# Kernel tuning notes

Measured on AMD Instinct MI355X. Metric: run time of the kernel, lower is better.

The kernel has to match this reference:

```python
import jax, jax.numpy as jnp
import numpy as np

NEG_SLOPE = 0.2  # DGL GATConv default leaky_relu slope


def gat_conv(x, src, dst, W, attn_l, attn_r, bias, res_W):
    """DGL GATConv (eval mode, residual=True with linear res_fc, bias).
    x: [N, F_in]; src/dst: [E]; W: [F_in, H*D]; attn_l/r: [H, D];
    bias: [H*D]; res_W: [F_in, H*D]. Returns [N, H, D]."""
    N = x.shape[0]
    H, D = attn_l.shape
    feat = (x @ W).reshape(N, H, D)
    el = jnp.sum(feat * attn_l, axis=-1)  # [N, H]
    er = jnp.sum(feat * attn_r, axis=-1)  # [N, H]
    e = jax.nn.leaky_relu(el[src] + er[dst], NEG_SLOPE)  # [E, H]
    # edge softmax over incoming edges of each dst node (numerically stable)
    m = jnp.full((N, H), -jnp.inf, dtype=e.dtype).at[dst].max(e)
    ex = jnp.exp(e - m[dst])
    s = jnp.zeros((N, H), dtype=e.dtype).at[dst].add(ex)
    alpha = ex / s[dst]  # [E, H]
    # scatter-aggregate messages alpha * feat[src] into dst
    rst = jnp.zeros((N, H, D), dtype=x.dtype).at[dst].add(alpha[:, :, None] * feat[src])
    rst = rst + (x @ res_W).reshape(N, H, D) + bias.reshape(1, H, D)
    return rst


def setup_inputs() -> dict:
    key = jax.random.key(0)
    N, E, F_IN, HID, OUT, H = 20000, 320000, 128, 128, 128, 4
    ks = jax.random.split(key, 32)
    ki = iter(range(32))

    def rn(shape, scale=0.05):
        return jax.random.normal(ks[next(ki)], shape, dtype=jnp.float32) * scale

    inp = {
        "n_feat": jax.random.normal(ks[next(ki)], (N, F_IN), dtype=jnp.float32),
        "src": jax.random.randint(ks[next(ki)], (E,), 0, N, dtype=jnp.int32),
        "dst": jax.random.randint(ks[next(ki)], (E,), 0, N, dtype=jnp.int32),
        # input GATConv: F_IN -> H x HID
        "W0": rn((F_IN, H * HID)), "al0": rn((H, HID)), "ar0": rn((H, HID)),
        "b0": rn((H * HID,)), "rW0": rn((F_IN, H * HID)),
        "DW0": rn((H * HID, HID)), "Db0": rn((HID,)),
        # middle GATConv: HID -> H x HID
        "W1": rn((HID, H * HID)), "al1": rn((H, HID)), "ar1": rn((H, HID)),
        "b1": rn((H * HID,)), "rW1": rn((HID, H * HID)),
        "DW1": rn((H * HID, HID)), "Db1": rn((HID,)),
        # output GATConv: HID -> H x OUT
        "W2": rn((HID, H * OUT)), "al2": rn((H, OUT)), "ar2": rn((H, OUT)),
        "b2": rn((H * OUT,)), "rW2": rn((HID, H * OUT)),
    }
    return inp


def reference(n_feat, src, dst,
              W0, al0, ar0, b0, rW0, DW0, Db0,
              W1, al1, ar1, b1, rW1, DW1, Db1,
              W2, al2, ar2, b2, rW2):
    N = n_feat.shape[0]
    relu = jax.nn.relu
    # input GAT block
    h = relu(gat_conv(n_feat, src, dst, W0, al0, ar0, b0, rW0))  # [N, H, HID]
    h = relu(h.reshape(N, -1) @ DW0 + Db0)                        # [N, HID]
    # middle GAT block
    h = relu(gat_conv(h, src, dst, W1, al1, ar1, b1, rW1))
    h = relu(h.reshape(N, -1) @ DW1 + Db1)
    # output GAT + head-mean + graph max pooling (single graph)
    h = relu(gat_conv(h, src, dst, W2, al2, ar2, b2, rW2))        # [N, H, OUT]
    h = relu(jnp.mean(h, axis=-2))                                 # [N, OUT]
    return jnp.max(h, axis=0, keepdims=True)                       # [1, OUT]
```

## Files before the change

kernel.cpp:

```cpp
#include <hip/hip_runtime.h>
#include <hip/hip_bf16.h>


typedef __attribute__((ext_vector_type(8))) short bf16x8;
typedef __attribute__((ext_vector_type(4))) float f32x4;
typedef __hip_bfloat16 bf16_t;

__device__ __forceinline__ unsigned int pack_bf16(float lo, float hi) {
  return (((unsigned int)__bfloat16_as_ushort(__float2bfloat16(hi))) << 16) |
         (unsigned int)__bfloat16_as_ushort(__float2bfloat16(lo));
}

__device__ __forceinline__ void gload_lds16(const void* g, void* l) {
  __builtin_amdgcn_global_load_lds(
      (const __attribute__((address_space(1))) void*)g,
      (__attribute__((address_space(3))) void*)l, 16, 0, 0);
}

__global__ __launch_bounds__(256) void mega_prep(
    const float* __restrict__ W0, const float* __restrict__ rW0,
    const float* __restrict__ W1, const float* __restrict__ rW1,
    const float* __restrict__ W2, const float* __restrict__ rW2,
    const float* __restrict__ DW0, const float* __restrict__ DW1,
    const float* __restrict__ al0, const float* __restrict__ ar0,
    const float* __restrict__ al1, const float* __restrict__ ar1,
    const float* __restrict__ al2, const float* __restrict__ ar2,
    const float* __restrict__ n_feat, bf16_t* __restrict__ wts,
    float* __restrict__ ALR, bf16_t* __restrict__ xbf,
    int* __restrict__ counts, float* __restrict__ d_out_f, int N) {
  __shared__ float tile[32][33];
  int b = blockIdx.x, tid = threadIdx.x;
  int r = tid >> 5, c = tid & 31;

  if (b < 384) {
    int mat = b >> 6;
    int t = b & 63;
    int kt = t >> 4, nt = t & 15;
    int L = mat >> 1, isR = mat & 1;
    const float* S = (L == 0) ? (isR ? rW0 : W0)
                   : (L == 1) ? (isR ? rW1 : W1) : (isR ? rW2 : W2);
    bf16_t* D = wts + L * 131072 + isR * 65536;
#pragma unroll
    for (int rr = 0; rr < 4; rr++)
      tile[r + rr * 8][c] = S[(kt * 32 + r + rr * 8) * 512 + nt * 32 + c];
    __syncthreads();
#pragma unroll
    for (int rr = 0; rr < 4; rr++)
      D[(nt * 32 + r + rr * 8) * 128 + kt * 32 + c] =
          __float2bfloat16(tile[c][r + rr * 8]);
  } else if (b < 512) {
    int i = b - 384;
    int mat = i >> 6;
    int t = i & 63;
    int kt = t & 15, nt = t >> 4;
    const float* S = mat ? DW1 : DW0;
    bf16_t* D = wts + 393216 + mat * 65536;
#pragma unroll
    for (int rr = 0; rr < 4; rr++)
      tile[r + rr * 8][c] = S[(kt * 32 + r + rr * 8) * 128 + nt * 32 + c];
    __syncthreads();
#pragma unroll
    for (int rr = 0; rr < 4; rr++)
      D[(nt * 32 + r + rr * 8) * 512 + kt * 32 + c] =
          __float2bfloat16(tile[c][r + rr * 8]);
  } else if (b < 524) {
    int idx = (b - 512) * 256 + tid;
    if (idx < 3072) {
      int L = idx >> 10;
      int k = (idx >> 3) & 127;
      int cc = idx & 7;
      int h = cc & 3;
      const float* W = (L == 0) ? W0 : (L == 1) ? W1 : W2;
      const float* a = (cc < 4) ? ((L == 0) ? al0 : (L == 1) ? al1 : al2)
                                : ((L == 0) ? ar0 : (L == 1) ? ar1 : ar2);
      float s = 0.f;
      for (int d = 0; d < 128; d++) s += W[k * 512 + h * 128 + d] * a[h * 128 + d];
      ALR[idx] = s;
    }
  } else if (b < 3024) {
    int i = ((b - 524) * 256 + tid) * 4;
    if (i < N * 128) {
      float4 v = *(const float4*)(n_feat + i);
      xbf[i + 0] = __float2bfloat16(v.x);
      xbf[i + 1] = __float2bfloat16(v.y);
      xbf[i + 2] = __float2bfloat16(v.z);
      xbf[i + 3] = __float2bfloat16(v.w);
    }
  } else {
    for (int i = tid; i < N; i += 256) counts[i] = 0;
    if (tid < 128) d_out_f[tid] = 0.f;
  }
}

__global__ __launch_bounds__(256) void gemm128el(
    const bf16_t* __restrict__ A, const bf16_t* __restrict__ Bt,
    const float* __restrict__ ALRl, bf16_t* __restrict__ C,
    float* __restrict__ el, float* __restrict__ er, int M, int ldc, int K) {
  __shared__ bf16_t As[128 * 64];
  __shared__ bf16_t Bs[128 * 64];
  int tid = threadIdx.x;
  int rowBase = blockIdx.y * 128;

  if (blockIdx.x == 8) {
    float* sALR = (float*)As;
#pragma unroll
    for (int j = 0; j < 4; j++) sALR[tid * 4 + j] = ALRl[tid * 4 + j];
    __syncthreads();
    int row = rowBase + (tid >> 1);
    int half = tid & 1;
    if (row < M) {
      const bf16_t* xr = A + (size_t)row * K + half * 64;
      float s[8] = {};
#pragma unroll
      for (int g = 0; g < 8; g++) {
        bf16x8 v = *(const bf16x8*)(xr + g * 8);
#pragma unroll
        for (int e = 0; e < 8; e++) {
          float f = __uint_as_float(((unsigned int)(unsigned short)v[e]) << 16);
          const float* Ak = sALR + (half * 64 + g * 8 + e) * 8;
#pragma unroll
          for (int cc = 0; cc < 8; cc++) s[cc] += f * Ak[cc];
        }
      }
#pragma unroll
      for (int cc = 0; cc < 8; cc++) s[cc] += __shfl_xor(s[cc], 1);
      if (half == 0)
        *(float4*)(el + row * 4) = make_float4(s[0], s[1], s[2], s[3]);
      else
        *(float4*)(er + row * 4) = make_float4(s[4], s[5], s[6], s[7]);
    }
    return;
  }

  int lane = tid & 63, wave = tid >> 6;
  int q = lane >> 4, r16 = lane & 15;
  int wm = (wave >> 1) * 64, wn = (wave & 1) * 64;
  int colBase = blockIdx.x * 128;

  f32x4 acc[4][4] = {};

  for (int k0 = 0; k0 < K; k0 += 64) {
#pragma unroll
    for (int p = 0; p < 4; p++) {
      int slotb = (wave * 4 + p) * 64;
      int s = slotb + lane;
      int r = s >> 3;
      int c = (s & 7) ^ (r & 7);
      int gr = rowBase + r;
      if (gr > M - 1) gr = M - 1;
      gload_lds16(A + (size_t)gr * K + k0 + c * 8, (char*)As + (size_t)slotb * 16);
      gload_lds16(Bt + (size_t)(colBase + r) * K + k0 + c * 8,
                  (char*)Bs + (size_t)slotb * 16);
    }
    __syncthreads();
#pragma unroll
    for (int ks = 0; ks < 64; ks += 32) {
      int koff = ks >> 3;
      bf16x8 af[4], bfr[4];
#pragma unroll
      for (int i = 0; i < 4; i++) {
        int R = wm + i * 16 + r16;
        int slot = R * 8 + ((q + koff) ^ (R & 7));
        af[i] = *(const bf16x8*)((const char*)As + (size_t)slot * 16);
      }
#pragma unroll
      for (int j = 0; j < 4; j++) {
        int R = wn + j * 16 + r16;
        int slot = R * 8 + ((q + koff) ^ (R & 7));
        bfr[j] = *(const bf16x8*)((const char*)Bs + (size_t)slot * 16);
      }
#pragma unroll
      for (int i = 0; i < 4; i++)
#pragma unroll
        for (int j = 0; j < 4; j++)
          acc[i][j] = __builtin_amdgcn_mfma_f32_16x16x32_bf16(af[i], bfr[j], acc[i][j], 0, 0, 0);
    }
    __syncthreads();
  }

  int odd = lane & 1;
  int colb0 = r16 & ~1;
#pragma unroll
  for (int i = 0; i < 4; i++) {
#pragma unroll
    for (int r = 0; r < 4; r++) {
      int row = rowBase + wm + i * 16 + q * 4 + r;
#pragma unroll
      for (int jp = 0; jp < 2; jp++) {
        float a0 = acc[i][2 * jp][r];
        float a1 = acc[i][2 * jp + 1][r];
        float p0 = __shfl_xor(a0, 1);
        float p1 = __shfl_xor(a1, 1);
        float lo = odd ? p1 : a0;
        float hi = odd ? a1 : p0;
        int col = colBase + wn + (2 * jp + odd) * 16 + colb0;
        if (row < M)
          *(unsigned int*)(C + (size_t)row * ldc + col) = pack_bf16(lo, hi);
      }
    }
  }
}

__global__ __launch_bounds__(256) void mfma_gemm64(
    const bf16_t* __restrict__ A, const bf16_t* __restrict__ Bt,
    const float* __restrict__ bias, bf16_t* __restrict__ C,
    int M, int ldc, int K) {
  __shared__ bf16_t As[64 * 64];
  __shared__ bf16_t Bs[64 * 64];
  int tid = threadIdx.x;
  int lane = tid & 63, wave = tid >> 6;
  int q = lane >> 4, r16 = lane & 15;
  int wm = (wave >> 1) * 32, wn = (wave & 1) * 32;
  int rowBase = blockIdx.y * 64, colBase = blockIdx.x * 64;

  f32x4 acc[2][2] = {};

  for (int k0 = 0; k0 < K; k0 += 64) {
#pragma unroll
    for (int p = 0; p < 2; p++) {
      int slotb = (wave * 2 + p) * 64;
      int s = slotb + lane;
      int r = s >> 3;
      int c = (s & 7) ^ (r & 7);
      int gr = rowBase + r;
      if (gr > M - 1) gr = M - 1;
      gload_lds16(A + (size_t)gr * K + k0 + c * 8, (char*)As + (size_t)slotb * 16);
      gload_lds16(Bt + (size_t)(colBase + r) * K + k0 + c * 8,
                  (char*)Bs + (size_t)slotb * 16);
    }
    __syncthreads();
#pragma unroll
    for (int ks = 0; ks < 64; ks += 32) {
      int koff = ks >> 3;
      bf16x8 af[2], bfr[2];
#pragma unroll
      for (int i = 0; i < 2; i++) {
        int R = wm + i * 16 + r16;
        int slot = R * 8 + ((q + koff) ^ (R & 7));
        af[i] = *(const bf16x8*)((const char*)As + (size_t)slot * 16);
      }
#pragma unroll
      for (int j = 0; j < 2; j++) {
        int R = wn + j * 16 + r16;
        int slot = R * 8 + ((q + koff) ^ (R & 7));
        bfr[j] = *(const bf16x8*)((const char*)Bs + (size_t)slot * 16);
      }
#pragma unroll
      for (int i = 0; i < 2; i++)
#pragma unroll
        for (int j = 0; j < 2; j++)
          acc[i][j] = __builtin_amdgcn_mfma_f32_16x16x32_bf16(af[i], bfr[j], acc[i][j], 0, 0, 0);
    }
    __syncthreads();
  }

  int odd = lane & 1;
  int colb0 = r16 & ~1;
#pragma unroll
  for (int i = 0; i < 2; i++) {
#pragma unroll
    for (int r = 0; r < 4; r++) {
      int row = rowBase + wm + i * 16 + q * 4 + r;
      float a0 = acc[i][0][r];
      float a1 = acc[i][1][r];
      float p0 = __shfl_xor(a0, 1);
      float p1 = __shfl_xor(a1, 1);
      float lo = odd ? p1 : a0;
      float hi = odd ? a1 : p0;
      int col = colBase + wn + odd * 16 + colb0;
      if (row < M) {
        float o0 = fmaxf(lo + bias[col], 0.f);
        float o1 = fmaxf(hi + bias[col + 1], 0.f);
        *(unsigned int*)(C + (size_t)row * ldc + col) = pack_bf16(o0, o1);
      }
    }
  }
}

__global__ __launch_bounds__(256) void count_kernel(const int* __restrict__ dst,
                                                    int* __restrict__ counts, int E) {
  int i = blockIdx.x * blockDim.x + threadIdx.x;
  if (i < E) atomicAdd(&counts[dst[i]], 1);
}

__global__ __launch_bounds__(1024) void scan_kernel(const int* __restrict__ counts,
                                                    int* __restrict__ row_ptr,
                                                    int* __restrict__ cursor, int N) {
  __shared__ int sums[1024];
  int t = threadIdx.x;
  int chunk = (N + 1023) / 1024;
  int begin = t * chunk;
  int end = begin + chunk;
  if (end > N) end = N;
  int s = 0;
  for (int i = begin; i < end; i++) s += counts[i];
  sums[t] = s;
  __syncthreads();
  for (int off = 1; off < 1024; off <<= 1) {
    int v = (t >= off) ? sums[t - off] : 0;
    __syncthreads();
    sums[t] += v;
    __syncthreads();
  }
  int run = (t == 0) ? 0 : sums[t - 1];
  for (int i = begin; i < end; i++) {
    row_ptr[i] = run;
    cursor[i] = run;
    run += counts[i];
  }
  if (t == 1023) row_ptr[N] = sums[1023];
}

__global__ __launch_bounds__(256) void scatter_kernel(
    const int* __restrict__ src, const int* __restrict__ dst,
    int* __restrict__ cursor, int* __restrict__ edge_src, int E) {
  int i = blockIdx.x * blockDim.x + threadIdx.x;
  if (i < E) {
    int d = dst[i];
    int pos = atomicAdd(&cursor[d], 1);
    edge_src[pos] = src[i];
  }
}

__global__ __launch_bounds__(256) void gat_agg_kernel(
    const bf16_t* __restrict__ fused,
    const float* __restrict__ el, const float* __restrict__ er,
    const float* __restrict__ bias, const int* __restrict__ row_ptr,
    const int* __restrict__ edge_src, bf16_t* __restrict__ out, int N) {
  int n = blockIdx.x;
  int h = threadIdx.x >> 6;
  int l = threadIdx.x & 63;
  int g = l >> 3, t = l & 7;
  int start = row_ptr[n];
  int deg = row_ptr[n + 1] - start;
  float er_nh = er[n * 4 + h];

  float acc[16] = {};
  float ssum = 0.f;
  const bf16_t* fbase = fused + h * 128 + t * 16;
  for (int i = g; i < deg; i += 8) {
    int s = edge_src[start + i];
    float e = el[s * 4 + h] + er_nh;
    e = (e > 0.f) ? e : 0.2f * e;
    float w = __expf(e);
    ssum += w;
    const bf16_t* fp = fbase + (size_t)s * 1024;
    uint4 f0 = *(const uint4*)(fp);
    uint4 f1 = *(const uint4*)(fp + 8);
    unsigned int u[8] = {f0.x, f0.y, f0.z, f0.w, f1.x, f1.y, f1.z, f1.w};
#pragma unroll
    for (int j = 0; j < 8; j++) {
      acc[2 * j] += w * __uint_as_float(u[j] << 16);
      acc[2 * j + 1] += w * __uint_as_float(u[j] & 0xffff0000u);
    }
  }
#pragma unroll
  for (int off = 8; off <= 32; off <<= 1) {
    ssum += __shfl_xor(ssum, off);
#pragma unroll
    for (int d = 0; d < 16; d++) acc[d] += __shfl_xor(acc[d], off);
  }

  if (g == 0) {
    float inv = (deg > 0) ? 1.f / ssum : 0.f;
    const bf16_t* rp = fused + (size_t)n * 1024 + 512 + h * 128 + t * 16;
    uint4 r0 = *(const uint4*)(rp);
    uint4 r1 = *(const uint4*)(rp + 8);
    unsigned int ru[8] = {r0.x, r0.y, r0.z, r0.w, r1.x, r1.y, r1.z, r1.w};
    const float* bp = bias + h * 128 + t * 16;
    unsigned int ow[8];
#pragma unroll
    for (int j = 0; j < 8; j++) {
      float o0 = fmaxf(acc[2 * j] * inv + __uint_as_float(ru[j] << 16) + bp[2 * j], 0.f);
      float o1 = fmaxf(acc[2 * j + 1] * inv + __uint_as_float(ru[j] & 0xffff0000u) + bp[2 * j + 1], 0.f);
      ow[j] = pack_bf16(o0, o1);
    }
    bf16_t* op = out + (size_t)n * 512 + h * 128 + t * 16;
    *(uint4*)(op) = make_uint4(ow[0], ow[1], ow[2], ow[3]);
    *(uint4*)(op + 8) = make_uint4(ow[4], ow[5], ow[6], ow[7]);
  }
}

__global__ __launch_bounds__(128) void pool_kernel(const bf16_t* __restrict__ g,
                                                   float* __restrict__ out, int N) {
  int d = threadIdx.x;
  float mx = 0.f;
  for (int n = blockIdx.x; n < N; n += gridDim.x) {
    const bf16_t* p = g + (size_t)n * 512 + d;
    float v = 0.25f * (__bfloat162float(p[0]) + __bfloat162float(p[128]) +
                       __bfloat162float(p[256]) + __bfloat162float(p[384]));
    mx = fmaxf(mx, v);
  }
  atomicMax((int*)out + d, __float_as_int(mx));
}

extern "C" void kernel_launch(void* const* d_in, const int* in_sizes, int n_in,
                              void* d_out, int out_size, void* d_ws, size_t ws_size,
                              hipStream_t stream) {
  const float* n_feat = (const float*)d_in[0];
  const int* src = (const int*)d_in[1];
  const int* dst = (const int*)d_in[2];
  const float* W0 = (const float*)d_in[3];
  const float* al0 = (const float*)d_in[4];
  const float* ar0 = (const float*)d_in[5];
  const float* b0 = (const float*)d_in[6];
  const float* rW0 = (const float*)d_in[7];
  const float* DW0 = (const float*)d_in[8];
  const float* Db0 = (const float*)d_in[9];
  const float* W1 = (const float*)d_in[10];
  const float* al1 = (const float*)d_in[11];
  const float* ar1 = (const float*)d_in[12];
  const float* b1 = (const float*)d_in[13];
  const float* rW1 = (const float*)d_in[14];
  const float* DW1 = (const float*)d_in[15];
  const float* Db1 = (const float*)d_in[16];
  const float* W2 = (const float*)d_in[17];
  const float* al2 = (const float*)d_in[18];
  const float* ar2 = (const float*)d_in[19];
  const float* b2 = (const float*)d_in[20];
  const float* rW2 = (const float*)d_in[21];

  const int N = in_sizes[0] / 128;
  const int E = in_sizes[1];

  bf16_t* xbf = (bf16_t*)d_ws;
  bf16_t* fusedFR = xbf + (size_t)N * 128;
  bf16_t* outC = fusedFR + (size_t)N * 1024;
  bf16_t* denseD = outC + (size_t)N * 512;
  bf16_t* wts = denseD + (size_t)N * 128;
  float* ALR = (float*)(wts + 524288);
  float* el = ALR + 3072;
  float* er = el + (size_t)N * 4;
  int* counts = (int*)(er + (size_t)N * 4);
  int* row_ptr = counts + N;
  int* cursor = row_ptr + (N + 1);
  int* edge_src = cursor + N;

  bf16_t* FW0 = wts;
  bf16_t* FW1 = wts + 131072;
  bf16_t* FW2 = wts + 262144;
  bf16_t* DWt0 = wts + 393216;
  bf16_t* DWt1 = wts + 458752;

  mega_prep<<<3025, 256, 0, stream>>>(
      W0, rW0, W1, rW1, W2, rW2, DW0, DW1,
      al0, ar0, al1, ar1, al2, ar2,
      n_feat, wts, ALR, xbf, counts, (float*)d_out, N);

  count_kernel<<<(E + 255) / 256, 256, 0, stream>>>(dst, counts, E);
  scan_kernel<<<1, 1024, 0, stream>>>(counts, row_ptr, cursor, N);
  scatter_kernel<<<(E + 255) / 256, 256, 0, stream>>>(src, dst, cursor, edge_src, E);

  dim3 gF(9, (N + 127) / 128);
  dim3 gD(2, (N + 63) / 64);

  gemm128el<<<gF, 256, 0, stream>>>(xbf, FW0, ALR, fusedFR, el, er, N, 1024, 128);
  gat_agg_kernel<<<N, 256, 0, stream>>>(fusedFR, el, er, b0, row_ptr, edge_src, outC, N);
  mfma_gemm64<<<gD, 256, 0, stream>>>(outC, DWt0, Db0, denseD, N, 128, 512);

  gemm128el<<<gF, 256, 0, stream>>>(denseD, FW1, ALR + 1024, fusedFR, el, er, N, 1024, 128);
  gat_agg_kernel<<<N, 256, 0, stream>>>(fusedFR, el, er, b1, row_ptr, edge_src, outC, N);
  mfma_gemm64<<<gD, 256, 0, stream>>>(outC, DWt1, Db1, denseD, N, 128, 512);

  gemm128el<<<gF, 256, 0, stream>>>(denseD, FW2, ALR + 2048, fusedFR, el, er, N, 1024, 128);
  gat_agg_kernel<<<N, 256, 0, stream>>>(fusedFR, el, er, b2, row_ptr, edge_src, outC, N);

  pool_kernel<<<256, 128, 0, stream>>>(outC, (float*)d_out, N);
}
```

Baseline: 451.7 us.

## Remap GAT aggregation so each wave gathers full 512-wide rows per edge

Changes the aggregation kernel's work split. Each wave now handles one edge at a time and loads the whole 1 KB feature row for all four heads as one coalesced 16-byte load per lane, instead of each wave covering one head with eight edge groups. Per-thread accumulators shrink from 16 to 8, and the cross-group shuffle reduction becomes a shared-memory reduction across the 4 waves followed by a 2-element-per-thread epilogue. It recomputes leaky-relu and exp per lane across 16 lanes per head, and it adds a block-wide barrier and shared-memory traffic.

```diff
diff --git a/kernel.cpp b/kernel.cpp
--- a/kernel.cpp
+++ b/kernel.cpp
@@ -327,58 +327,54 @@
     const float* __restrict__ el, const float* __restrict__ er,
     const float* __restrict__ bias, const int* __restrict__ row_ptr,
     const int* __restrict__ edge_src, bf16_t* __restrict__ out, int N) {
+  __shared__ float accL[4][64][8];
+  __shared__ float ssumL[4][4];
   int n = blockIdx.x;
-  int h = threadIdx.x >> 6;
-  int l = threadIdx.x & 63;
-  int g = l >> 3, t = l & 7;
+  int tid = threadIdx.x;
+  int wave = tid >> 6, lane = tid & 63;
+  int hh = lane >> 4;
   int start = row_ptr[n];
   int deg = row_ptr[n + 1] - start;
-  float er_nh = er[n * 4 + h];
-
-  float acc[16] = {};
+  float er_h = er[n * 4 + hh];
+
+  float acc[8] = {};
   float ssum = 0.f;
-  const bf16_t* fbase = fused + h * 128 + t * 16;
-  for (int i = g; i < deg; i += 8) {
+  const bf16_t* fbase = fused + (size_t)lane * 8;
+  for (int i = wave; i < deg; i += 4) {
     int s = edge_src[start + i];
-    float e = el[s * 4 + h] + er_nh;
+    float e = el[s * 4 + hh] + er_h;
     e = (e > 0.f) ? e : 0.2f * e;
     float w = __expf(e);
     ssum += w;
-    const bf16_t* fp = fbase + (size_t)s * 1024;
-    uint4 f0 = *(const uint4*)(fp);
-    uint4 f1 = *(const uint4*)(fp + 8);
-    unsigned int u[8] = {f0.x, f0.y, f0.z, f0.w, f1.x, f1.y, f1.z, f1.w};
-#pragma unroll
-    for (int j = 0; j < 8; j++) {
+    uint4 f = *(const uint4*)(fbase + (size_t)s * 1024);
+    unsigned int u[4] = {f.x, f.y, f.z, f.w};
+#pragma unroll
+    for (int j = 0; j < 4; j++) {
       acc[2 * j] += w * __uint_as_float(u[j] << 16);
       acc[2 * j + 1] += w * __uint_as_float(u[j] & 0xffff0000u);
     }
   }
-#pragma unroll
-  for (int off = 8; off <= 32; off <<= 1) {
-    ssum += __shfl_xor(ssum, off);
-#pragma unroll
-    for (int d = 0; d < 16; d++) acc[d] += __shfl_xor(acc[d], off);
-  }
-
-  if (g == 0) {
-    float inv = (deg > 0) ? 1.f / ssum : 0.f;
-    const bf16_t* rp = fused + (size_t)n * 1024 + 512 + h * 128 + t * 16;
-    uint4 r0 = *(const uint4*)(rp);
-    uint4 r1 = *(const uint4*)(rp + 8);
-    unsigned int ru[8] = {r0.x, r0.y, r0.z, r0.w, r1.x, r1.y, r1.z, r1.w};
-    const float* bp = bias + h * 128 + t * 16;
-    unsigned int ow[8];
-#pragma unroll
-    for (int j = 0; j < 8; j++) {
-      float o0 = fmaxf(acc[2 * j] * inv + __uint_as_float(ru[j] << 16) + bp[2 * j], 0.f);
-      float o1 = fmaxf(acc[2 * j + 1] * inv + __uint_as_float(ru[j] & 0xffff0000u) + bp[2 * j + 1], 0.f);
-      ow[j] = pack_bf16(o0, o1);
-    }
-    bf16_t* op = out + (size_t)n * 512 + h * 128 + t * 16;
-    *(uint4*)(op) = make_uint4(ow[0], ow[1], ow[2], ow[3]);
-    *(uint4*)(op + 8) = make_uint4(ow[4], ow[5], ow[6], ow[7]);
-  }
+  *(float4*)&accL[wave][lane][0] = make_float4(acc[0], acc[1], acc[2], acc[3]);
+  *(float4*)&accL[wave][lane][4] = make_float4(acc[4], acc[5], acc[6], acc[7]);
+  if ((lane & 15) == 0) ssumL[wave][hh] = ssum;
+  __syncthreads();
+
+  int d = tid * 2;
+  int l = d >> 3, j = d & 7;
+  float a0 = 0.f, a1 = 0.f;
+#pragma unroll
+  for (int w = 0; w < 4; w++) {
+    a0 += accL[w][l][j];
+    a1 += accL[w][l][j + 1];
+  }
+  int h = tid >> 6;
+  float ssum4 = ssumL[0][h] + ssumL[1][h] + ssumL[2][h] + ssumL[3][h];
+  float inv = (deg > 0) ? 1.f / ssum4 : 0.f;
+  unsigned int ru = *(const unsigned int*)(fused + (size_t)n * 1024 + 512 + d);
+  float2 bv = *(const float2*)(bias + d);
+  float o0 = fmaxf(a0 * inv + __uint_as_float(ru << 16) + bv.x, 0.f);
+  float o1 = fmaxf(a1 * inv + __uint_as_float(ru & 0xffff0000u) + bv.y, 0.f);
+  *(unsigned int*)(out + (size_t)n * 512 + d) = pack_bf16(o0, o1);
 }
 
 __global__ __launch_bounds__(128) void pool_kernel(const bf16_t* __restrict__ g,
```

Result: no change. 444.9 us (-1.5%).
